# Kernel optimization log

Hardware: AMD Instinct MI355X
Metric: run time of the kernel (lower is better)

Reference implementation:

```python
import jax, jax.numpy as jnp
import numpy as np

N_NODES = 50000
N_EDGES = 800000
N_GRAPHS = 64
NEG_SLOPE = 0.2  # PyG GATv2Conv default negative_slope
LN_EPS = 1e-5


def gatv2(x, src, dst, Wl, bl, Wr, br, att, bias, heads, out_ch, concat):
    """Faithful eval-mode PyG GATv2Conv: x_l=lin_l(x) (source), x_r=lin_r(x) (target),
    e = att . leaky_relu(x_l[src] + x_r[dst]), segment-softmax over dst, scatter-add."""
    N = x.shape[0]
    H, C = heads, out_ch
    xl = (x @ Wl + bl).reshape(N, H, C)
    xr = (x @ Wr + br).reshape(N, H, C)
    e = jax.nn.leaky_relu(xl[src] + xr[dst], NEG_SLOPE)        # [E, H, C]
    logits = jnp.einsum('ehc,hc->eh', e, att)                  # [E, H]
    m = jax.ops.segment_max(logits, dst, num_segments=N)       # every node has a self-loop
    ex = jnp.exp(logits - m[dst])
    denom = jax.ops.segment_sum(ex, dst, num_segments=N)
    alpha = ex / (denom[dst] + 1e-16)                          # [E, H]
    out = jax.ops.segment_sum(xl[src] * alpha[..., None], dst, num_segments=N)  # [N, H, C]
    out = out.reshape(N, H * C) if concat else out.mean(axis=1)
    return out + bias


def setup_inputs() -> dict:
    key = jax.random.key(0)
    ks = jax.random.split(key, 32)

    def g(i, shape):  # glorot-ish
        scale = np.sqrt(2.0 / (shape[0] + shape[-1]))
        return (jax.random.normal(ks[i], shape, jnp.float32) * scale)

    inp = {
        'x': jax.random.normal(ks[0], (N_NODES, 4), jnp.float32),
        'edge_index': jax.random.randint(ks[1], (2, N_EDGES), 0, N_NODES, dtype=jnp.int64),
        'batch': jnp.sort(jax.random.randint(ks[2], (N_NODES,), 0, N_GRAPHS, dtype=jnp.int64)),
        # conv1: 4 -> 64, heads=4, concat -> 256
        'W1l': g(3, (4, 256)), 'b1l': jnp.zeros((256,), jnp.float32),
        'W1r': g(4, (4, 256)), 'b1r': jnp.zeros((256,), jnp.float32),
        'a1': g(5, (4, 64)), 'c1b': jnp.zeros((256,), jnp.float32),
        # conv2: 256 -> 64, heads=2, concat -> 128
        'W2l': g(6, (256, 128)), 'b2l': jnp.zeros((128,), jnp.float32),
        'W2r': g(7, (256, 128)), 'b2r': jnp.zeros((128,), jnp.float32),
        'a2': g(8, (2, 64)), 'c2b': jnp.zeros((128,), jnp.float32),
        # conv3: 128 -> 256, heads=1, concat=False -> 256
        'W3l': g(9, (128, 256)), 'b3l': jnp.zeros((256,), jnp.float32),
        'W3r': g(10, (128, 256)), 'b3r': jnp.zeros((256,), jnp.float32),
        'a3': g(11, (1, 256)), 'c3b': jnp.zeros((256,), jnp.float32),
        # enhancer MLP + LayerNorm
        'We1': g(12, (256, 512)), 'be1': jnp.zeros((512,), jnp.float32),
        'We2': g(13, (512, 256)), 'be2': jnp.zeros((256,), jnp.float32),
        'lng': jnp.ones((256,), jnp.float32), 'lnb': jnp.zeros((256,), jnp.float32),
    }
    return inp


def reference(x, edge_index, batch,
              W1l, b1l, W1r, b1r, a1, c1b,
              W2l, b2l, W2r, b2r, a2, c2b,
              W3l, b3l, W3r, b3r, a3, c3b,
              We1, be1, We2, be2, lng, lnb):
    N = x.shape[0]
    loop = jnp.arange(N, dtype=edge_index.dtype)  # add_self_loops=True (PyG default)
    src = jnp.concatenate([edge_index[0], loop])
    dst = jnp.concatenate([edge_index[1], loop])

    h = jax.nn.relu(gatv2(x, src, dst, W1l, b1l, W1r, b1r, a1, c1b, 4, 64, True))
    h = jax.nn.relu(gatv2(h, src, dst, W2l, b2l, W2r, b2r, a2, c2b, 2, 64, True))
    h = gatv2(h, src, dst, W3l, b3l, W3r, b3r, a3, c3b, 1, 256, False)

    # global mean pool per graph
    sums = jax.ops.segment_sum(h, batch, num_segments=N_GRAPHS)          # [G, 256]
    cnt = jax.ops.segment_sum(jnp.ones((N, 1), h.dtype), batch, num_segments=N_GRAPHS)
    pooled = sums / jnp.maximum(cnt, 1.0)

    # enhancer (dropout off in eval): Linear -> ReLU -> Linear -> LayerNorm
    z = jax.nn.relu(pooled @ We1 + be1) @ We2 + be2
    mu = z.mean(axis=-1, keepdims=True)
    var = z.var(axis=-1, keepdims=True)
    return (z - mu) / jnp.sqrt(var + LN_EPS) * lng + lnb
```

## Files before the change

### kernel.cpp

```cpp
#include <hip/hip_runtime.h>
#include <hip/hip_bf16.h>
#include <math.h>

#define NN 50000
#define NE0 800000
#define ETOT (NE0 + NN)
#define NG 64
#define SCAN_BLKS ((NN + 63) / 64)
#define DMAX_THR 8.0f

typedef __bf16 bf16x8 __attribute__((ext_vector_type(8)));
typedef float  f32x4  __attribute__((ext_vector_type(4)));

__device__ __forceinline__ float bf2f(unsigned short u) {
    return __uint_as_float(((unsigned)u) << 16);
}
__device__ __forceinline__ unsigned short f2bf(float f) {
    unsigned u = __float_as_uint(f);
    return (unsigned short)((u + 0x7FFFu + ((u >> 16) & 1u)) >> 16);
}

__device__ __forceinline__ void edge_sd(const int* __restrict__ ei, int e, int& s, int& d) {
    if (e < NE0) { s = ei[e]; d = ei[NE0 + e]; }
    else { s = e - NE0; d = s; }
}

__global__ __launch_bounds__(256)
void hist_dst(const int* __restrict__ ei, int* __restrict__ deg) {
    int e = blockIdx.x * blockDim.x + threadIdx.x;
    if (e >= ETOT) return;
    int s, d; edge_sd(ei, e, s, d); (void)s;
    atomicAdd(&deg[d], 1);
}

__global__ __launch_bounds__(64)
void scan1(const int* __restrict__ deg, int* __restrict__ psum) {
    int i = blockIdx.x * 64 + threadIdx.x;
    int v = (i < NN) ? deg[i] : 0;
#pragma unroll
    for (int off = 1; off < 64; off <<= 1) {
        int t = __shfl_up(v, off);
        if ((int)threadIdx.x >= off) v += t;
    }
    if (threadIdx.x == 63) psum[blockIdx.x] = v;
}

__global__ __launch_bounds__(1024)
void scan2(int* __restrict__ psum) {
    __shared__ int sm[1024];
    int t = threadIdx.x;
    sm[t] = (t < SCAN_BLKS) ? psum[t] : 0;
    __syncthreads();
    for (int off = 1; off < 1024; off <<= 1) {
        int v = (t >= off) ? sm[t - off] : 0;
        __syncthreads();
        sm[t] += v;
        __syncthreads();
    }
    if (t < SCAN_BLKS) psum[t] = (t == 0) ? 0 : sm[t - 1];
}

__global__ __launch_bounds__(64)
void scan3(const int* __restrict__ deg, const int* __restrict__ psum,
           int* __restrict__ rowptr) {
    int i = blockIdx.x * 64 + threadIdx.x;
    int v = (i < NN) ? deg[i] : 0;
    int inc = v;
#pragma unroll
    for (int off = 1; off < 64; off <<= 1) {
        int t = __shfl_up(inc, off);
        if ((int)threadIdx.x >= off) inc += t;
    }
    int excl = inc - v + psum[blockIdx.x];
    if (i < NN) rowptr[i] = excl;
    if (i == NN - 1) rowptr[NN] = excl + v;
}

__global__ __launch_bounds__(256)
void scatter_csr(const int* __restrict__ ei, int* __restrict__ cursor,
                 int* __restrict__ col) {
    int e = blockIdx.x * blockDim.x + threadIdx.x;
    if (e >= ETOT) return;
    int s, d; edge_sd(ei, e, s, d);
    int pos = atomicAdd(&cursor[d], 1);
    col[pos] = s;
}

template<int KIN, int NOUT>
__global__ __launch_bounds__(256)
void wfrag_prep(const float* __restrict__ W, unsigned short* __restrict__ Wf) {
    constexpr int KB = KIN / 32;
    int tid = blockIdx.x * 256 + threadIdx.x;
    if (tid >= KIN * NOUT) return;
    int j = tid & 7;
    int l = (tid >> 3) & 63;
    int rest = tid >> 9;
    int kb = rest % KB, t = rest / KB;
    int k = kb * 32 + (l >> 4) * 8 + j;
    int colj = t * 16 + (l & 15);
    Wf[tid] = f2bf(W[(size_t)k * NOUT + colj]);
}

__global__ __launch_bounds__(256)
void gat1_fused(const float* __restrict__ x,
                const int* __restrict__ rowptr, const int* __restrict__ col,
                const float* __restrict__ W1l, const float* __restrict__ b1l,
                const float* __restrict__ W1r, const float* __restrict__ b1r,
                const float* __restrict__ a1, const float* __restrict__ c1b,
                unsigned short* __restrict__ out) {
    int lane = threadIdx.x & 63;
    int wave0 = (blockIdx.x * blockDim.x + threadIdx.x) >> 6;
    int nwaves = (gridDim.x * blockDim.x) >> 6;
    int ch0 = lane * 4;

    float wl[4][4], wr[4][4];
#pragma unroll
    for (int k = 0; k < 4; ++k) {
        float4 l4 = *reinterpret_cast<const float4*>(W1l + k * 256 + ch0);
        wl[k][0] = l4.x; wl[k][1] = l4.y; wl[k][2] = l4.z; wl[k][3] = l4.w;
        float4 r4 = *reinterpret_cast<const float4*>(W1r + k * 256 + ch0);
        wr[k][0] = r4.x; wr[k][1] = r4.y; wr[k][2] = r4.z; wr[k][3] = r4.w;
    }
    float4 blv = *reinterpret_cast<const float4*>(b1l + ch0);
    float4 brv = *reinterpret_cast<const float4*>(b1r + ch0);
    float4 av  = *reinterpret_cast<const float4*>(a1 + ch0);
    float4 cbv = *reinterpret_cast<const float4*>(c1b + ch0);
    float bl[4] = { blv.x, blv.y, blv.z, blv.w };
    float ar[4] = { av.x, av.y, av.z, av.w };

    const float4* x4 = reinterpret_cast<const float4*>(x);

    for (int node = wave0; node < NN; node += nwaves) {
        float4 xn = x4[node];
        float blr[4];
#pragma unroll
        for (int p = 0; p < 4; ++p) {
            float xr = fmaf(xn.x, wr[0][p], fmaf(xn.y, wr[1][p],
                       fmaf(xn.z, wr[2][p], fmaf(xn.w, wr[3][p],
                       ((const float*)&brv)[p]))));
            blr[p] = bl[p] + xr;
        }
        float m = -INFINITY, l = 0.f;
        float ax = 0.f, ay = 0.f, az = 0.f, aw = 0.f;

        int beg = rowptr[node], end = rowptr[node + 1];
        int idx = beg;
        for (; idx + 3 < end; idx += 4) {
            float4 v[4];
            float dd[4];
#pragma unroll
            for (int q = 0; q < 4; ++q) v[q] = x4[col[idx + q]];
#pragma unroll
            for (int q = 0; q < 4; ++q) {
                float d = 0.f;
#pragma unroll
                for (int p = 0; p < 4; ++p) {
                    float u = fmaf(v[q].x, wl[0][p], fmaf(v[q].y, wl[1][p],
                              fmaf(v[q].z, wl[2][p], fmaf(v[q].w, wl[3][p], blr[p]))));
                    u = u > 0.f ? u : 0.2f * u;
                    d = fmaf(u, ar[p], d);
                }
                dd[q] = d;
            }
#pragma unroll
            for (int off = 8; off >= 1; off >>= 1) {
#pragma unroll
                for (int q = 0; q < 4; ++q) dd[q] += __shfl_xor(dd[q], off);
            }
            float pmax = fmaxf(fmaxf(dd[0], dd[1]), fmaxf(dd[2], dd[3]));
            if (pmax > m + DMAX_THR) {
                float sc = __expf(m - pmax);
                l *= sc; ax *= sc; ay *= sc; az *= sc; aw *= sc;
                m = pmax;
            }
            float p0 = __expf(dd[0] - m), p1 = __expf(dd[1] - m);
            float p2 = __expf(dd[2] - m), p3 = __expf(dd[3] - m);
            l += (p0 + p1) + (p2 + p3);
            ax += fmaf(p0, v[0].x, p1 * v[1].x) + fmaf(p2, v[2].x, p3 * v[3].x);
            ay += fmaf(p0, v[0].y, p1 * v[1].y) + fmaf(p2, v[2].y, p3 * v[3].y);
            az += fmaf(p0, v[0].z, p1 * v[1].z) + fmaf(p2, v[2].z, p3 * v[3].z);
            aw += fmaf(p0, v[0].w, p1 * v[1].w) + fmaf(p2, v[2].w, p3 * v[3].w);
        }
        for (; idx < end; ++idx) {
            float4 v0 = x4[col[idx]];
            float d0 = 0.f;
#pragma unroll
            for (int p = 0; p < 4; ++p) {
                float u0 = fmaf(v0.x, wl[0][p], fmaf(v0.y, wl[1][p],
                           fmaf(v0.z, wl[2][p], fmaf(v0.w, wl[3][p], blr[p]))));
                u0 = u0 > 0.f ? u0 : 0.2f * u0;
                d0 = fmaf(u0, ar[p], d0);
            }
#pragma unroll
            for (int off = 8; off >= 1; off >>= 1) d0 += __shfl_xor(d0, off);
            if (d0 > m + DMAX_THR) {
                float sc = __expf(m - d0);
                l *= sc; ax *= sc; ay *= sc; az *= sc; aw *= sc;
                m = d0;
            }
            float p0 = __expf(d0 - m);
            l += p0;
            ax = fmaf(p0, v0.x, ax);
            ay = fmaf(p0, v0.y, ay);
            az = fmaf(p0, v0.z, az);
            aw = fmaf(p0, v0.w, aw);
        }
        float inv = 1.f / (l + 1e-16f);
        unsigned short o[4];
#pragma unroll
        for (int p = 0; p < 4; ++p) {
            float v = fmaf(ax, wl[0][p], fmaf(ay, wl[1][p],
                      fmaf(az, wl[2][p], aw * wl[3][p]))) * inv
                      + bl[p] + ((const float*)&cbv)[p];
            o[p] = f2bf(fmaxf(v, 0.f));
        }
        *reinterpret_cast<ushort4*>(out + (size_t)node * 256 + ch0) =
            make_ushort4(o[0], o[1], o[2], o[3]);
    }
}

template<int KIN, int NOUT>
__global__ __launch_bounds__(256)
void gemm_mfma2(const unsigned short* __restrict__ X,
                const unsigned short* __restrict__ WfL, const float* __restrict__ bL,
                unsigned short* __restrict__ outL,
                const unsigned short* __restrict__ WfR, const float* __restrict__ bR,
                unsigned short* __restrict__ outR) {
    constexpr int KB = KIN / 32, NT = NOUT / 16;
    int lane = threadIdx.x & 63;
    int wv = threadIdx.x >> 6;
    int row0 = blockIdx.x * 64 + wv * 16;
    int r16 = lane & 15, kg = lane >> 4;

    int arow = row0 + r16; if (arow >= NN) arow = NN - 1;
    const unsigned short* xrow = X + (size_t)arow * KIN + kg * 8;
    bf16x8 af[KB];
#pragma unroll
    for (int kb = 0; kb < KB; ++kb)
        af[kb] = *reinterpret_cast<const bf16x8*>(xrow + kb * 32);

    const unsigned short* Wf[2] = { WfL, WfR };
    const float* bb[2] = { bL, bR };
    unsigned short* oo[2] = { outL, outR };

#pragma unroll
    for (int w = 0; w < 2; ++w) {
        const bf16x8* wbase = reinterpret_cast<const bf16x8*>(Wf[w]) + lane;
        const float* bw = bb[w];
        unsigned short* ow = oo[w];
#pragma unroll 1
        for (int t = 0; t < NT; ++t) {
            f32x4 acc = {0.f, 0.f, 0.f, 0.f};
            const bf16x8* wp = wbase + (size_t)t * KB * 64;
#pragma unroll
            for (int kb = 0; kb < KB; ++kb)
                acc = __builtin_amdgcn_mfma_f32_16x16x32_bf16(af[kb], wp[kb * 64], acc, 0, 0, 0);
            float bv = bw[t * 16 + r16];
#pragma unroll
            for (int rg = 0; rg < 4; ++rg) {
                int row = row0 + kg * 4 + rg;
                if (row < NN)
                    ow[(size_t)row * NOUT + t * 16 + r16] = f2bf(acc[rg] + bv);
            }
        }
    }
}

template<int H, int C, bool RELU, bool OUT_BF16>
__global__ __launch_bounds__(256)
void gat_fused(const unsigned short* __restrict__ xl, const unsigned short* __restrict__ xr,
               const int* __restrict__ rowptr, const int* __restrict__ col,
               const float* __restrict__ att, const float* __restrict__ bias,
               void* __restrict__ outv) {
    constexpr int HC = H * C;
    constexpr int CPL = HC / 64;
    constexpr int GRP = C / CPL;
    int lane = threadIdx.x & 63;
    int wave0 = (blockIdx.x * blockDim.x + threadIdx.x) >> 6;
    int nwaves = (gridDim.x * blockDim.x) >> 6;
    int ch0 = lane * CPL;

    float areg[CPL], breg[CPL];
#pragma unroll
    for (int p = 0; p < CPL; ++p) { areg[p] = att[ch0 + p]; breg[p] = bias[ch0 + p]; }

    for (int node = wave0; node < NN; node += nwaves) {
        float xrv[CPL];
        if constexpr (CPL == 4) {
            ushort4 u = *reinterpret_cast<const ushort4*>(xr + (size_t)node * HC + ch0);
            xrv[0] = bf2f(u.x); xrv[1] = bf2f(u.y); xrv[2] = bf2f(u.z); xrv[3] = bf2f(u.w);
        } else {
            ushort2 u = *reinterpret_cast<const ushort2*>(xr + (size_t)node * HC + ch0);
            xrv[0] = bf2f(u.x); xrv[1] = bf2f(u.y);
        }
        float m = -INFINITY, l = 0.f, acc[CPL];
#pragma unroll
        for (int p = 0; p < CPL; ++p) acc[p] = 0.f;

        int beg = rowptr[node], end = rowptr[node + 1];
        int idx = beg;
        for (; idx + 3 < end; idx += 4) {
            float a[4][CPL];
            float dd[4];
#pragma unroll
            for (int q = 0; q < 4; ++q) {
                int s = col[idx + q];
                if constexpr (CPL == 4) {
                    ushort4 u = *reinterpret_cast<const ushort4*>(xl + (size_t)s * HC + ch0);
                    a[q][0] = bf2f(u.x); a[q][1] = bf2f(u.y); a[q][2] = bf2f(u.z); a[q][3] = bf2f(u.w);
                } else {
                    ushort2 u = *reinterpret_cast<const ushort2*>(xl + (size_t)s * HC + ch0);
                    a[q][0] = bf2f(u.x); a[q][1] = bf2f(u.y);
                }
            }
#pragma unroll
            for (int q = 0; q < 4; ++q) {
                float d = 0.f;
#pragma unroll
                for (int p = 0; p < CPL; ++p) {
                    float v = a[q][p] + xrv[p];
                    v = v > 0.f ? v : 0.2f * v;
                    d = fmaf(v, areg[p], d);
                }
                dd[q] = d;
            }
#pragma unroll
            for (int off = GRP >> 1; off >= 1; off >>= 1) {
#pragma unroll
                for (int q = 0; q < 4; ++q) dd[q] += __shfl_xor(dd[q], off);
            }
            float pmax = fmaxf(fmaxf(dd[0], dd[1]), fmaxf(dd[2], dd[3]));
            if (pmax > m + DMAX_THR) {
                float sc = __expf(m - pmax);
                l *= sc;
#pragma unroll
                for (int p = 0; p < CPL; ++p) acc[p] *= sc;
                m = pmax;
            }
            float p0 = __expf(dd[0] - m), p1 = __expf(dd[1] - m);
            float p2 = __expf(dd[2] - m), p3 = __expf(dd[3] - m);
            l += (p0 + p1) + (p2 + p3);
#pragma unroll
            for (int p = 0; p < CPL; ++p)
                acc[p] += fmaf(p0, a[0][p], p1 * a[1][p]) + fmaf(p2, a[2][p], p3 * a[3][p]);
        }
        for (; idx < end; ++idx) {
            int s0 = col[idx];
            float a0[CPL];
            if constexpr (CPL == 4) {
                ushort4 u0 = *reinterpret_cast<const ushort4*>(xl + (size_t)s0 * HC + ch0);
                a0[0] = bf2f(u0.x); a0[1] = bf2f(u0.y); a0[2] = bf2f(u0.z); a0[3] = bf2f(u0.w);
            } else {
                ushort2 u0 = *reinterpret_cast<const ushort2*>(xl + (size_t)s0 * HC + ch0);
                a0[0] = bf2f(u0.x); a0[1] = bf2f(u0.y);
            }
            float d0 = 0.f;
#pragma unroll
            for (int p = 0; p < CPL; ++p) {
                float v0 = a0[p] + xrv[p];
                v0 = v0 > 0.f ? v0 : 0.2f * v0;
                d0 = fmaf(v0, areg[p], d0);
            }
#pragma unroll
            for (int off = GRP >> 1; off >= 1; off >>= 1) d0 += __shfl_xor(d0, off);
            if (d0 > m + DMAX_THR) {
                float sc = __expf(m - d0);
                l *= sc;
#pragma unroll
                for (int p = 0; p < CPL; ++p) acc[p] *= sc;
                m = d0;
            }
            float p0 = __expf(d0 - m);
            l += p0;
#pragma unroll
            for (int p = 0; p < CPL; ++p)
                acc[p] = fmaf(p0, a0[p], acc[p]);
        }
        float inv = 1.f / (l + 1e-16f);
        float o[CPL];
#pragma unroll
        for (int p = 0; p < CPL; ++p) {
            float v = acc[p] * inv + breg[p];
            if (RELU) v = fmaxf(v, 0.f);
            o[p] = v;
        }
        if constexpr (OUT_BF16) {
            unsigned short* out = (unsigned short*)outv;
            if constexpr (CPL == 4) {
                *reinterpret_cast<ushort4*>(out + (size_t)node * HC + ch0) =
                    make_ushort4(f2bf(o[0]), f2bf(o[1]), f2bf(o[2]), f2bf(o[3]));
            } else {
                *reinterpret_cast<ushort2*>(out + (size_t)node * HC + ch0) =
                    make_ushort2(f2bf(o[0]), f2bf(o[1]));
            }
        } else {
            float* out = (float*)outv;
            if constexpr (CPL == 4) {
                *reinterpret_cast<float4*>(out + (size_t)node * HC + ch0) =
                    make_float4(o[0], o[1], o[2], o[3]);
            } else {
                *reinterpret_cast<float2*>(out + (size_t)node * HC + ch0) =
                    make_float2(o[0], o[1]);
            }
        }
    }
}

__global__ __launch_bounds__(64)
void graph_bounds(const int* __restrict__ batch, float* __restrict__ cnt) {
    int g = threadIdx.x;
    if (g >= NG) return;
    int lo = 0, hi = NN;
    while (lo < hi) { int mid = (lo + hi) >> 1; if (batch[mid] < g) lo = mid + 1; else hi = mid; }
    int lo2 = lo, hi2 = NN;
    while (lo2 < hi2) { int mid = (lo2 + hi2) >> 1; if (batch[mid] < g + 1) lo2 = mid + 1; else hi2 = mid; }
    cnt[g] = (float)(lo2 - lo);
}

__global__ __launch_bounds__(256)
void pool_sum(const float* __restrict__ h, const int* __restrict__ batch,
              float* pooled) {
    __shared__ int gb[32];
    int c = threadIdx.x;
    int n0 = blockIdx.x * 32;
    int n1 = min(n0 + 32, NN);
    int cnt = n1 - n0;
    if (c < cnt) gb[c] = batch[n0 + c];
    __syncthreads();
    if (gb[0] == gb[cnt - 1]) {
        float acc = 0.f;
#pragma unroll 4
        for (int i = 0; i < cnt; ++i) acc += h[(size_t)(n0 + i) * 256 + c];
        atomicAdd(&pooled[gb[0] * 256 + c], acc);
    } else {
        int cur = gb[0]; float acc = 0.f;
        for (int i = 0; i < cnt; ++i) {
            int g = gb[i];
            if (g != cur) { atomicAdd(&pooled[cur * 256 + c], acc); acc = 0.f; cur = g; }
            acc += h[(size_t)(n0 + i) * 256 + c];
        }
        atomicAdd(&pooled[cur * 256 + c], acc);
    }
}

__global__ __launch_bounds__(256)
void mlp_ln(const float* __restrict__ pooled, const float* __restrict__ cnt,
            const float* __restrict__ We1, const float* __restrict__ be1,
            const float* __restrict__ We2, const float* __restrict__ be2,
            const float* __restrict__ lng, const float* __restrict__ lnb,
            float* __restrict__ out) {
    __shared__ float p[256];
    __shared__ float t[512];
    __shared__ float red[8];
    int g = blockIdx.x, tid = threadIdx.x;
    p[tid] = pooled[g * 256 + tid] / fmaxf(cnt[g], 1.0f);
    __syncthreads();
    for (int jj = tid; jj < 512; jj += 256) {
        float s = be1[jj];
        for (int k = 0; k < 256; ++k) s = fmaf(p[k], We1[(size_t)k * 512 + jj], s);
        t[jj] = fmaxf(s, 0.f);
    }
    __syncthreads();
    float z = be2[tid];
    for (int k = 0; k < 512; ++k) z = fmaf(t[k], We2[(size_t)k * 256 + tid], z);
    float sv = z, sq = z * z;
#pragma unroll
    for (int off = 32; off >= 1; off >>= 1) {
        sv += __shfl_xor(sv, off);
        sq += __shfl_xor(sq, off);
    }
    int wv = tid >> 6;
    if ((tid & 63) == 0) { red[wv] = sv; red[4 + wv] = sq; }
    __syncthreads();
    float tot = red[0] + red[1] + red[2] + red[3];
    float totq = red[4] + red[5] + red[6] + red[7];
    float mu = tot * (1.f / 256.f);
    float var = totq * (1.f / 256.f) - mu * mu;
    float r = rsqrtf(var + 1e-5f);
    out[g * 256 + tid] = (z - mu) * r * lng[tid] + lnb[tid];
}

extern "C" void kernel_launch(void* const* d_in, const int* in_sizes, int n_in,
                              void* d_out, int out_size, void* d_ws, size_t ws_size,
                              hipStream_t stream) {
    const float* x   = (const float*)d_in[0];
    const int*   ei  = (const int*)d_in[1];
    const int*   bat = (const int*)d_in[2];
    const float *W1l = (const float*)d_in[3], *b1l = (const float*)d_in[4];
    const float *W1r = (const float*)d_in[5], *b1r = (const float*)d_in[6];
    const float *a1  = (const float*)d_in[7], *c1b = (const float*)d_in[8];
    const float *W2l = (const float*)d_in[9],  *b2l = (const float*)d_in[10];
    const float *W2r = (const float*)d_in[11], *b2r = (const float*)d_in[12];
    const float *a2  = (const float*)d_in[13], *c2b = (const float*)d_in[14];
    const float *W3l = (const float*)d_in[15], *b3l = (const float*)d_in[16];
    const float *W3r = (const float*)d_in[17], *b3r = (const float*)d_in[18];
    const float *a3  = (const float*)d_in[19], *c3b = (const float*)d_in[20];
    const float *We1 = (const float*)d_in[21], *be1 = (const float*)d_in[22];
    const float *We2 = (const float*)d_in[23], *be2 = (const float*)d_in[24];
    const float *lng = (const float*)d_in[25], *lnb = (const float*)d_in[26];

    char* base = (char*)d_ws;
    size_t off = 0;
    auto nxt = [&](size_t bytes) { char* p = base + off; off = (off + bytes + 255) & ~(size_t)255; return p; };
    unsigned short* Abuf = (unsigned short*)nxt((size_t)NN * 256 * 2);
    unsigned short* Bbuf = (unsigned short*)nxt((size_t)NN * 256 * 2);
    unsigned short* Hb16 = (unsigned short*)nxt((size_t)NN * 256 * 2);
    float* Hb32 = (float*)nxt((size_t)NN * 256 * 4);
    int* deg    = (int*)nxt(NN * 4);
    int* rowptr = (int*)nxt((NN + 1) * 4);
    int* cursor = (int*)nxt(NN * 4);
    int* colv   = (int*)nxt((size_t)ETOT * 4);
    int* psum   = (int*)nxt(1024 * 4);
    float* POOL = (float*)nxt(NG * 256 * 4);
    float* CNT  = (float*)nxt(NG * 4);
    unsigned short* Wf2l = (unsigned short*)nxt(256 * 128 * 2);
    unsigned short* Wf2r = (unsigned short*)nxt(256 * 128 * 2);
    unsigned short* Wf3l = (unsigned short*)nxt(128 * 256 * 2);
    unsigned short* Wf3r = (unsigned short*)nxt(128 * 256 * 2);

    const int GEMM_BLKS = (NN + 63) / 64;
    const int GAT_BLKS = 3125;

    hipMemsetAsync(deg, 0, NN * sizeof(int), stream);
    hist_dst<<<(ETOT + 255) / 256, 256, 0, stream>>>(ei, deg);
    scan1<<<SCAN_BLKS, 64, 0, stream>>>(deg, psum);
    scan2<<<1, 1024, 0, stream>>>(psum);
    scan3<<<SCAN_BLKS, 64, 0, stream>>>(deg, psum, rowptr);
    hipMemcpyAsync(cursor, rowptr, NN * sizeof(int), hipMemcpyDeviceToDevice, stream);
    scatter_csr<<<(ETOT + 255) / 256, 256, 0, stream>>>(ei, cursor, colv);

    wfrag_prep<256, 128><<<(256 * 128 + 255) / 256, 256, 0, stream>>>(W2l, Wf2l);
    wfrag_prep<256, 128><<<(256 * 128 + 255) / 256, 256, 0, stream>>>(W2r, Wf2r);
    wfrag_prep<128, 256><<<(128 * 256 + 255) / 256, 256, 0, stream>>>(W3l, Wf3l);
    wfrag_prep<128, 256><<<(128 * 256 + 255) / 256, 256, 0, stream>>>(W3r, Wf3r);

    gat1_fused<<<GAT_BLKS, 256, 0, stream>>>(x, rowptr, colv, W1l, b1l, W1r, b1r, a1, c1b, Hb16);

    gemm_mfma2<256, 128><<<GEMM_BLKS, 256, 0, stream>>>(Hb16, Wf2l, b2l, Abuf, Wf2r, b2r, Bbuf);
    gat_fused<2, 64, true, true><<<GAT_BLKS, 256, 0, stream>>>(Abuf, Bbuf, rowptr, colv, a2, c2b, Hb16);

    gemm_mfma2<128, 256><<<GEMM_BLKS, 256, 0, stream>>>(Hb16, Wf3l, b3l, Abuf, Wf3r, b3r, Bbuf);
    gat_fused<1, 256, false, false><<<GAT_BLKS, 256, 0, stream>>>(Abuf, Bbuf, rowptr, colv, a3, c3b, Hb32);

    hipMemsetAsync(POOL, 0, (size_t)NG * 256 * 4, stream);
    graph_bounds<<<1, 64, 0, stream>>>(bat, CNT);
    pool_sum<<<(NN + 31) / 32, 256, 0, stream>>>(Hb32, bat, POOL);
    mlp_ln<<<NG, 256, 0, stream>>>(POOL, CNT, We1, be1, We2, be2, lng, lnb, (float*)d_out);
}
```

Before: 488.2 us.

## Pad CSR rows to multiples of eight and process edges in masked 8-wide batches

Each node's CSR row is padded to a multiple of 8 entries, with the padding zero-filled so it points at node 0. The GAT aggregation kernels then run a single 8-wide unrolled loop with masked logits instead of a 4-wide loop plus a scalar tail. The online-softmax rescale becomes branchless. The aim is more gathers in flight per iteration and an end to the divergent tail. In exchange, every node now does wasted gathers and exponentials on padding (average degree is about 17), and the 3.4MB colv buffer gets an extra memset.

```diff
diff --git a/kernel.cpp b/kernel.cpp
--- a/kernel.cpp
+++ b/kernel.cpp
@@ -5,6 +5,7 @@
 #define NN 50000
 #define NE0 800000
 #define ETOT (NE0 + NN)
+#define ETOTP (ETOT + NN * 7)
 #define NG 64
 #define SCAN_BLKS ((NN + 63) / 64)
 #define DMAX_THR 8.0f
@@ -23,6 +24,14 @@
 __device__ __forceinline__ void edge_sd(const int* __restrict__ ei, int e, int& s, int& d) {
     if (e < NE0) { s = ei[e]; d = ei[NE0 + e]; }
     else { s = e - NE0; d = s; }
+}
+
+__device__ __forceinline__ float max8(const float* d) {
+    return fmaxf(fmaxf(fmaxf(d[0], d[1]), fmaxf(d[2], d[3])),
+                 fmaxf(fmaxf(d[4], d[5]), fmaxf(d[6], d[7])));
+}
+__device__ __forceinline__ float sum8(const float* p) {
+    return ((p[0] + p[1]) + (p[2] + p[3])) + ((p[4] + p[5]) + (p[6] + p[7]));
 }
 
 __global__ __launch_bounds__(256)
@@ -36,7 +45,7 @@
 __global__ __launch_bounds__(64)
 void scan1(const int* __restrict__ deg, int* __restrict__ psum) {
     int i = blockIdx.x * 64 + threadIdx.x;
-    int v = (i < NN) ? deg[i] : 0;
+    int v = (i < NN) ? ((deg[i] + 7) & ~7) : 0;
 #pragma unroll
     for (int off = 1; off < 64; off <<= 1) {
         int t = __shfl_up(v, off);
@@ -64,7 +73,7 @@
 void scan3(const int* __restrict__ deg, const int* __restrict__ psum,
            int* __restrict__ rowptr) {
     int i = blockIdx.x * 64 + threadIdx.x;
-    int v = (i < NN) ? deg[i] : 0;
+    int v = (i < NN) ? ((deg[i] + 7) & ~7) : 0;
     int inc = v;
 #pragma unroll
     for (int off = 1; off < 64; off <<= 1) {
@@ -103,7 +112,8 @@
 
 __global__ __launch_bounds__(256)
 void gat1_fused(const float* __restrict__ x,
-                const int* __restrict__ rowptr, const int* __restrict__ col,
+                const int* __restrict__ rowptr, const int* __restrict__ deg,
+                const int* __restrict__ col,
                 const float* __restrict__ W1l, const float* __restrict__ b1l,
                 const float* __restrict__ W1r, const float* __restrict__ b1r,
                 const float* __restrict__ a1, const float* __restrict__ c1b,
@@ -143,15 +153,20 @@
         float m = -INFINITY, l = 0.f;
         float ax = 0.f, ay = 0.f, az = 0.f, aw = 0.f;
 
-        int beg = rowptr[node], end = rowptr[node + 1];
-        int idx = beg;
-        for (; idx + 3 < end; idx += 4) {
-            float4 v[4];
-            float dd[4];
-#pragma unroll
-            for (int q = 0; q < 4; ++q) v[q] = x4[col[idx + q]];
-#pragma unroll
-            for (int q = 0; q < 4; ++q) {
+        int beg = rowptr[node];
+        int npad = rowptr[node + 1] - beg;
+        int nreal = deg[node];
+        const int* cp = col + beg;
+        for (int idx = 0; idx < npad; idx += 8) {
+            int cs[8];
+#pragma unroll
+            for (int q = 0; q < 8; ++q) cs[q] = cp[idx + q];
+            float4 v[8];
+#pragma unroll
+            for (int q = 0; q < 8; ++q) v[q] = x4[cs[q]];
+            float dd[8];
+#pragma unroll
+            for (int q = 0; q < 8; ++q) {
                 float d = 0.f;
 #pragma unroll
                 for (int p = 0; p < 4; ++p) {
@@ -165,45 +180,31 @@
 #pragma unroll
             for (int off = 8; off >= 1; off >>= 1) {
 #pragma unroll
-                for (int q = 0; q < 4; ++q) dd[q] += __shfl_xor(dd[q], off);
-            }
-            float pmax = fmaxf(fmaxf(dd[0], dd[1]), fmaxf(dd[2], dd[3]));
-            if (pmax > m + DMAX_THR) {
-                float sc = __expf(m - pmax);
-                l *= sc; ax *= sc; ay *= sc; az *= sc; aw *= sc;
-                m = pmax;
-            }
-            float p0 = __expf(dd[0] - m), p1 = __expf(dd[1] - m);
-            float p2 = __expf(dd[2] - m), p3 = __expf(dd[3] - m);
-            l += (p0 + p1) + (p2 + p3);
-            ax += fmaf(p0, v[0].x, p1 * v[1].x) + fmaf(p2, v[2].x, p3 * v[3].x);
-            ay += fmaf(p0, v[0].y, p1 * v[1].y) + fmaf(p2, v[2].y, p3 * v[3].y);
-            az += fmaf(p0, v[0].z, p1 * v[1].z) + fmaf(p2, v[2].z, p3 * v[3].z);
-            aw += fmaf(p0, v[0].w, p1 * v[1].w) + fmaf(p2, v[2].w, p3 * v[3].w);
-        }
-        for (; idx < end; ++idx) {
-            float4 v0 = x4[col[idx]];
-            float d0 = 0.f;
-#pragma unroll
-            for (int p = 0; p < 4; ++p) {
-                float u0 = fmaf(v0.x, wl[0][p], fmaf(v0.y, wl[1][p],
-                           fmaf(v0.z, wl[2][p], fmaf(v0.w, wl[3][p], blr[p]))));
-                u0 = u0 > 0.f ? u0 : 0.2f * u0;
-                d0 = fmaf(u0, ar[p], d0);
-            }
-#pragma unroll
-            for (int off = 8; off >= 1; off >>= 1) d0 += __shfl_xor(d0, off);
-            if (d0 > m + DMAX_THR) {
-                float sc = __expf(m - d0);
-                l *= sc; ax *= sc; ay *= sc; az *= sc; aw *= sc;
-                m = d0;
-            }
-            float p0 = __expf(d0 - m);
-            l += p0;
-            ax = fmaf(p0, v0.x, ax);
-            ay = fmaf(p0, v0.y, ay);
-            az = fmaf(p0, v0.z, az);
-            aw = fmaf(p0, v0.w, aw);
+                for (int q = 0; q < 8; ++q) dd[q] += __shfl_xor(dd[q], off);
+            }
+            int nrem = nreal - idx;
+#pragma unroll
+            for (int q = 0; q < 8; ++q) if (q >= nrem) dd[q] = -INFINITY;
+            float pmax = max8(dd);
+            float nm = (pmax > m + DMAX_THR) ? pmax : m;
+            float sc = __expf(m - nm);
+            m = nm;
+            float p[8];
+#pragma unroll
+            for (int q = 0; q < 8; ++q) p[q] = __expf(dd[q] - m);
+            l = fmaf(l, sc, sum8(p));
+            float sx = (fmaf(p[0], v[0].x, p[1] * v[1].x) + fmaf(p[2], v[2].x, p[3] * v[3].x))
+                     + (fmaf(p[4], v[4].x, p[5] * v[5].x) + fmaf(p[6], v[6].x, p[7] * v[7].x));
+            float sy = (fmaf(p[0], v[0].y, p[1] * v[1].y) + fmaf(p[2], v[2].y, p[3] * v[3].y))
+                     + (fmaf(p[4], v[4].y, p[5] * v[5].y) + fmaf(p[6], v[6].y, p[7] * v[7].y));
+            float sz = (fmaf(p[0], v[0].z, p[1] * v[1].z) + fmaf(p[2], v[2].z, p[3] * v[3].z))
+                     + (fmaf(p[4], v[4].z, p[5] * v[5].z) + fmaf(p[6], v[6].z, p[7] * v[7].z));
+            float sw = (fmaf(p[0], v[0].w, p[1] * v[1].w) + fmaf(p[2], v[2].w, p[3] * v[3].w))
+                     + (fmaf(p[4], v[4].w, p[5] * v[5].w) + fmaf(p[6], v[6].w, p[7] * v[7].w));
+            ax = fmaf(ax, sc, sx);
+            ay = fmaf(ay, sc, sy);
+            az = fmaf(az, sc, sz);
+            aw = fmaf(aw, sc, sw);
         }
         float inv = 1.f / (l + 1e-16f);
         unsigned short o[4];
@@ -269,7 +270,8 @@
 template<int H, int C, bool RELU, bool OUT_BF16>
 __global__ __launch_bounds__(256)
 void gat_fused(const unsigned short* __restrict__ xl, const unsigned short* __restrict__ xr,
-               const int* __restrict__ rowptr, const int* __restrict__ col,
+               const int* __restrict__ rowptr, const int* __restrict__ deg,
+               const int* __restrict__ col,
                const float* __restrict__ att, const float* __restrict__ bias,
                void* __restrict__ outv) {
     constexpr int HC = H * C;
@@ -297,24 +299,28 @@
 #pragma unroll
         for (int p = 0; p < CPL; ++p) acc[p] = 0.f;
 
-        int beg = rowptr[node], end = rowptr[node + 1];
-        int idx = beg;
-        for (; idx + 3 < end; idx += 4) {
-            float a[4][CPL];
-            float dd[4];
-#pragma unroll
-            for (int q = 0; q < 4; ++q) {
-                int s = col[idx + q];
+        int beg = rowptr[node];
+        int npad = rowptr[node + 1] - beg;
+        int nreal = deg[node];
+        const int* cp = col + beg;
+        for (int idx = 0; idx < npad; idx += 8) {
+            int cs[8];
+#pragma unroll
+            for (int q = 0; q < 8; ++q) cs[q] = cp[idx + q];
+            float a[8][CPL];
+#pragma unroll
+            for (int q = 0; q < 8; ++q) {
                 if constexpr (CPL == 4) {
-                    ushort4 u = *reinterpret_cast<const ushort4*>(xl + (size_t)s * HC + ch0);
+                    ushort4 u = *reinterpret_cast<const ushort4*>(xl + (size_t)cs[q] * HC + ch0);
                     a[q][0] = bf2f(u.x); a[q][1] = bf2f(u.y); a[q][2] = bf2f(u.z); a[q][3] = bf2f(u.w);
                 } else {
-                    ushort2 u = *reinterpret_cast<const ushort2*>(xl + (size_t)s * HC + ch0);
+                    ushort2 u = *reinterpret_cast<const ushort2*>(xl + (size_t)cs[q] * HC + ch0);
                     a[q][0] = bf2f(u.x); a[q][1] = bf2f(u.y);
                 }
             }
-#pragma unroll
-            for (int q = 0; q < 4; ++q) {
+            float dd[8];
+#pragma unroll
+            for (int q = 0; q < 8; ++q) {
                 float d = 0.f;
 #pragma unroll
                 for (int p = 0; p < CPL; ++p) {
@@ -327,54 +333,25 @@
 #pragma unroll
             for (int off = GRP >> 1; off >= 1; off >>= 1) {
 #pragma unroll
-                for (int q = 0; q < 4; ++q) dd[q] += __shfl_xor(dd[q], off);
-            }
-            float pmax = fmaxf(fmaxf(dd[0], dd[1]), fmaxf(dd[2], dd[3]));
-            if (pmax > m + DMAX_THR) {
-                float sc = __expf(m - pmax);
-                l *= sc;
-#pragma unroll
-                for (int p = 0; p < CPL; ++p) acc[p] *= sc;
-                m = pmax;
-            }
-            float p0 = __expf(dd[0] - m), p1 = __expf(dd[1] - m);
-            float p2 = __expf(dd[2] - m), p3 = __expf(dd[3] - m);
-            l += (p0 + p1) + (p2 + p3);
-#pragma unroll
-            for (int p = 0; p < CPL; ++p)
-                acc[p] += fmaf(p0, a[0][p], p1 * a[1][p]) + fmaf(p2, a[2][p], p3 * a[3][p]);
-        }
-        for (; idx < end; ++idx) {
-            int s0 = col[idx];
-            float a0[CPL];
-            if constexpr (CPL == 4) {
-                ushort4 u0 = *reinterpret_cast<const ushort4*>(xl + (size_t)s0 * HC + ch0);
-                a0[0] = bf2f(u0.x); a0[1] = bf2f(u0.y); a0[2] = bf2f(u0.z); a0[3] = bf2f(u0.w);
-            } else {
-                ushort2 u0 = *reinterpret_cast<const ushort2*>(xl + (size_t)s0 * HC + ch0);
-                a0[0] = bf2f(u0.x); a0[1] = bf2f(u0.y);
-            }
-            float d0 = 0.f;
-#pragma unroll
-            for (int p = 0; p < CPL; ++p) {
-                float v0 = a0[p] + xrv[p];
-                v0 = v0 > 0.f ? v0 : 0.2f * v0;
-                d0 = fmaf(v0, areg[p], d0);
-            }
-#pragma unroll
-            for (int off = GRP >> 1; off >= 1; off >>= 1) d0 += __shfl_xor(d0, off);
-            if (d0 > m + DMAX_THR) {
-                float sc = __expf(m - d0);
-                l *= sc;
-#pragma unroll
-                for (int p = 0; p < CPL; ++p) acc[p] *= sc;
-                m = d0;
-            }
-            float p0 = __expf(d0 - m);
-            l += p0;
-#pragma unroll
-            for (int p = 0; p < CPL; ++p)
-                acc[p] = fmaf(p0, a0[p], acc[p]);
+                for (int q = 0; q < 8; ++q) dd[q] += __shfl_xor(dd[q], off);
+            }
+            int nrem = nreal - idx;
+#pragma unroll
+            for (int q = 0; q < 8; ++q) if (q >= nrem) dd[q] = -INFINITY;
+            float pmax = max8(dd);
+            float nm = (pmax > m + DMAX_THR) ? pmax : m;
+            float sc = __expf(m - nm);
+            m = nm;
+            float p[8];
+#pragma unroll
+            for (int q = 0; q < 8; ++q) p[q] = __expf(dd[q] - m);
+            l = fmaf(l, sc, sum8(p));
+#pragma unroll
+            for (int pc = 0; pc < CPL; ++pc) {
+                float s = (fmaf(p[0], a[0][pc], p[1] * a[1][pc]) + fmaf(p[2], a[2][pc], p[3] * a[3][pc]))
+                        + (fmaf(p[4], a[4][pc], p[5] * a[5][pc]) + fmaf(p[6], a[6][pc], p[7] * a[7][pc]));
+                acc[pc] = fmaf(acc[pc], sc, s);
+            }
         }
         float inv = 1.f / (l + 1e-16f);
         float o[CPL];
@@ -509,7 +486,7 @@
     int* deg    = (int*)nxt(NN * 4);
     int* rowptr = (int*)nxt((NN + 1) * 4);
     int* cursor = (int*)nxt(NN * 4);
-    int* colv   = (int*)nxt((size_t)ETOT * 4);
+    int* colv   = (int*)nxt((size_t)ETOTP * 4);
     int* psum   = (int*)nxt(1024 * 4);
     float* POOL = (float*)nxt(NG * 256 * 4);
     float* CNT  = (float*)nxt(NG * 4);
@@ -522,6 +499,7 @@
     const int GAT_BLKS = 3125;
 
     hipMemsetAsync(deg, 0, NN * sizeof(int), stream);
+    hipMemsetAsync(colv, 0, (size_t)ETOTP * sizeof(int), stream);
     hist_dst<<<(ETOT + 255) / 256, 256, 0, stream>>>(ei, deg);
     scan1<<<SCAN_BLKS, 64, 0, stream>>>(deg, psum);
     scan2<<<1, 1024, 0, stream>>>(psum);
@@ -534,13 +512,13 @@
     wfrag_prep<128, 256><<<(128 * 256 + 255) / 256, 256, 0, stream>>>(W3l, Wf3l);
     wfrag_prep<128, 256><<<(128 * 256 + 255) / 256, 256, 0, stream>>>(W3r, Wf3r);
 
-    gat1_fused<<<GAT_BLKS, 256, 0, stream>>>(x, rowptr, colv, W1l, b1l, W1r, b1r, a1, c1b, Hb16);
+    gat1_fused<<<GAT_BLKS, 256, 0, stream>>>(x, rowptr, deg, colv, W1l, b1l, W1r, b1r, a1, c1b, Hb16);
 
     gemm_mfma2<256, 128><<<GEMM_BLKS, 256, 0, stream>>>(Hb16, Wf2l, b2l, Abuf, Wf2r, b2r, Bbuf);
-    gat_fused<2, 64, true, true><<<GAT_BLKS, 256, 0, stream>>>(Abuf, Bbuf, rowptr, colv, a2, c2b, Hb16);
+    gat_fused<2, 64, true, true><<<GAT_BLKS, 256, 0, stream>>>(Abuf, Bbuf, rowptr, deg, colv, a2, c2b, Hb16);
 
     gemm_mfma2<128, 256><<<GEMM_BLKS, 256, 0, stream>>>(Hb16, Wf3l, b3l, Abuf, Wf3r, b3r, Bbuf);
-    gat_fused<1, 256, false, false><<<GAT_BLKS, 256, 0, stream>>>(Abuf, Bbuf, rowptr, colv, a3, c3b, Hb32);
+    gat_fused<1, 256, false, false><<<GAT_BLKS, 256, 0, stream>>>(Abuf, Bbuf, rowptr, deg, colv, a3, c3b, Hb32);
 
     hipMemsetAsync(POOL, 0, (size_t)NG * 256 * 4, stream);
     graph_bounds<<<1, 64, 0, stream>>>(bat, CNT);
```

Result: slower. 547.8 us (+12.2%).
